# Performance work log

Measured on AMD Instinct MI355X. Metric: run time of the kernel, lower is better.

Reference implementation:

```python
import jax, jax.numpy as jnp
import numpy as np

N_NODES = 50000
N_EDGES = 800000
IN_DIM = 128
HID = 256
BN_EPS = 1e-5
NEG_SLOPE = 0.01


def setup_inputs() -> dict:
    key = jax.random.key(0)
    ks = jax.random.split(key, 8)
    inp = {
        "x": jax.random.normal(ks[0], (N_NODES, IN_DIM), dtype=jnp.float32),
        "src": jax.random.randint(ks[1], (N_EDGES,), 0, N_NODES, dtype=jnp.int32),
        "dst": jax.random.randint(ks[2], (N_EDGES,), 0, N_NODES, dtype=jnp.int32),
        # layer 0 MLP (in->hid->hid) + BN params
        "w1_0": jax.random.normal(ks[3], (IN_DIM, HID), dtype=jnp.float32) / np.sqrt(IN_DIM),
        "b1_0": jnp.zeros((HID,), jnp.float32),
        "w2_0": jax.random.normal(ks[4], (HID, HID), dtype=jnp.float32) / np.sqrt(HID),
        "b2_0": jnp.zeros((HID,), jnp.float32),
        "g0": jnp.ones((HID,), jnp.float32),
        "be0": jnp.zeros((HID,), jnp.float32),
        "m0": jnp.zeros((HID,), jnp.float32),
        "v0": jnp.ones((HID,), jnp.float32),
        # layers 1..2 stacked (hid->hid->hid) + BN params
        "w1_r": jax.random.normal(ks[5], (2, HID, HID), dtype=jnp.float32) / np.sqrt(HID),
        "b1_r": jnp.zeros((2, HID), jnp.float32),
        "w2_r": jax.random.normal(ks[6], (2, HID, HID), dtype=jnp.float32) / np.sqrt(HID),
        "b2_r": jnp.zeros((2, HID), jnp.float32),
        "g_r": jnp.ones((2, HID), jnp.float32),
        "be_r": jnp.zeros((2, HID), jnp.float32),
        "m_r": jnp.zeros((2, HID), jnp.float32),
        "v_r": jnp.ones((2, HID), jnp.float32),
    }
    return inp


def _gin_layer(h, src, dst, w1, b1, w2, b2, g, be, m, v, last):
    # GINConv (eps=0): (1+eps)*h + sum_{j in N(i)} h_j  via gather + scatter-add
    agg = jax.ops.segment_sum(h[src], dst, num_segments=N_NODES)
    z = h + agg
    # 2-layer MLP (dropout is identity in eval)
    z = jax.nn.leaky_relu(z @ w1 + b1, NEG_SLOPE)
    z = z @ w2 + b2
    # BatchNorm1d (eval: running stats)
    z = (z - m) * jax.lax.rsqrt(v + BN_EPS) * g + be
    if not last:
        z = jax.nn.leaky_relu(z, NEG_SLOPE)
    return z


def reference(x, src, dst, w1_0, b1_0, w2_0, b2_0, g0, be0, m0, v0,
              w1_r, b1_r, w2_r, b2_r, g_r, be_r, m_r, v_r):
    h = _gin_layer(x, src, dst, w1_0, b1_0, w2_0, b2_0, g0, be0, m0, v0, last=False)
    for l in range(2):
        h = _gin_layer(h, src, dst, w1_r[l], b1_r[l], w2_r[l], b2_r[l],
                       g_r[l], be_r[l], m_r[l], v_r[l], last=(l == 1))
    return h
```

## Files before the change

### kernel.cpp

```cpp
#include <hip/hip_runtime.h>
#include <hip/hip_bf16.h>
#include <stdint.h>

#define NN 50000
#define NE 800000
#define IND 128
#define HID 256
#define MPAD 50048
#define NBLK 49

#define NCH 64
#define CHSZ 12500
#define NRG 8
#define RGSZ 6250

typedef unsigned int uint32;
typedef unsigned short ushort_t;
typedef __attribute__((ext_vector_type(8))) short short8;
typedef __attribute__((ext_vector_type(4))) float f32x4;

typedef const __attribute__((address_space(1))) void* gptr_t;
typedef __attribute__((address_space(3))) void* lptr_t;

__device__ __forceinline__ ushort_t f2b(float f) {
  uint32 u = __float_as_uint(f);
  u = (u + 0x7fffu + ((u >> 16) & 1u)) >> 16;
  return (ushort_t)u;
}
__device__ __forceinline__ float blo(uint32 u) { return __uint_as_float(u << 16); }
__device__ __forceinline__ float bhi(uint32 u) { return __uint_as_float(u & 0xffff0000u); }
__device__ __forceinline__ uint32 pack2(float a, float b) {
  return (uint32)f2b(a) | ((uint32)f2b(b) << 16);
}

__global__ __launch_bounds__(256) void histp_k(const int* __restrict__ dst,
                                               uint32* __restrict__ partial,
                                               int* __restrict__ rnk) {
  __shared__ uint32 lh[RGSZ];
  const int c = blockIdx.x & (NCH - 1);
  const int rg = blockIdx.x >> 6;
  const int r0 = rg * RGSZ;
  for (int i = threadIdx.x; i < RGSZ; i += 256) lh[i] = 0;
  __syncthreads();
  const int e0 = c * CHSZ;
  for (int i = threadIdx.x; i < CHSZ; i += 256) {
    int e = e0 + i;
    int d = dst[e] - r0;
    if ((unsigned)d < (unsigned)RGSZ) rnk[e] = (int)atomicAdd(&lh[d], 1u);
  }
  __syncthreads();
  uint32* po = partial + (size_t)c * NN + r0;
  for (int i = threadIdx.x; i < RGSZ; i += 256) po[i] = lh[i];
}

__global__ void coff_k(uint32* __restrict__ partial, int* __restrict__ cnt) {
  int bin = blockIdx.x * 256 + threadIdx.x;
  if (bin >= NN) return;
  uint32 run = 0;
#pragma unroll
  for (int c = 0; c < NCH; c++) {
    uint32 t = partial[(size_t)c * NN + bin];
    partial[(size_t)c * NN + bin] = run;
    run += t;
  }
  cnt[bin] = (int)run;
}

__global__ void bsum_k(const int* __restrict__ cnt, int* __restrict__ bsum) {
  __shared__ int ws[16];
  const int tid = threadIdx.x, ln = tid & 63, wv = tid >> 6;
  int i = blockIdx.x * 1024 + tid;
  int v = (i < NN) ? cnt[i] : 0;
#pragma unroll
  for (int d = 32; d; d >>= 1) v += __shfl_down(v, d, 64);
  if (ln == 0) ws[wv] = v;
  __syncthreads();
  if (tid < 16) {
    int s = ws[tid];
#pragma unroll
    for (int d = 8; d; d >>= 1) s += __shfl_down(s, d, 64);
    if (tid == 0) bsum[blockIdx.x] = s;
  }
}

__global__ void bscan_k(int* __restrict__ bsum, int* __restrict__ rp) {
  int tid = threadIdx.x;
  int v = (tid < NBLK) ? bsum[tid] : 0;
  int x = v;
#pragma unroll
  for (int d = 1; d < 64; d <<= 1) {
    int t = __shfl_up(x, d, 64);
    if (tid >= d) x += t;
  }
  if (tid < NBLK) bsum[tid] = x - v;
  if (tid == 0) rp[NN] = NE;
}

__global__ void scan2_k(const int* __restrict__ cnt, const int* __restrict__ bsum,
                        int* __restrict__ rp) {
  __shared__ int ws[16];
  const int tid = threadIdx.x, ln = tid & 63, wv = tid >> 6;
  int i = blockIdx.x * 1024 + tid;
  int v = (i < NN) ? cnt[i] : 0;
  int x = v;
#pragma unroll
  for (int d = 1; d < 64; d <<= 1) {
    int t = __shfl_up(x, d, 64);
    if (ln >= d) x += t;
  }
  if (ln == 63) ws[wv] = x;
  __syncthreads();
  if (tid < 16) {
    int s = ws[tid];
#pragma unroll
    for (int d = 1; d < 16; d <<= 1) {
      int t = __shfl_up(s, d, 64);
      if (tid >= d) s += t;
    }
    ws[tid] = s;
  }
  __syncthreads();
  int excl = x - v + (wv ? ws[wv - 1] : 0) + bsum[blockIdx.x];
  if (i < NN) rp[i] = excl;
}

__global__ void scat2_k(const int* __restrict__ src, const int* __restrict__ dst,
                        const int* __restrict__ rp, const uint32* __restrict__ partial,
                        const int* __restrict__ rnk, int* __restrict__ esrc) {
  int e = blockIdx.x * 256 + threadIdx.x;
  if (e < NE) {
    int d = dst[e];
    int c = e / CHSZ;
    int pos = rp[d] + (int)partial[(size_t)c * NN + d] + rnk[e];
    esrc[pos] = src[e];
  }
}

__global__ void prep_k(const float* __restrict__ w1_0, const float* __restrict__ w2_0,
                       const float* __restrict__ w1_r, const float* __restrict__ w2_r,
                       const float* b1_0, const float* b2_0, const float* g0,
                       const float* be0, const float* m0, const float* v0,
                       const float* b1_r, const float* b2_r, const float* g_r,
                       const float* be_r, const float* m_r, const float* v_r,
                       ushort_t* __restrict__ wt,
                       float* bi1, float* sc2, float* bi2) {
  const int which = blockIdx.y;
  if (which < 6) {
    const int n = blockIdx.x, k = threadIdx.x;
    const float* w; ushort_t* o; int K = HID;
    switch (which) {
      case 0: w = w1_0; o = wt; K = IND; break;
      case 1: w = w2_0; o = wt + HID * IND; break;
      case 2: w = w1_r; o = wt + HID * IND + 1 * HID * HID; break;
      case 3: w = w2_r; o = wt + HID * IND + 2 * HID * HID; break;
      case 4: w = w1_r + HID * HID; o = wt + HID * IND + 3 * HID * HID; break;
      default: w = w2_r + HID * HID; o = wt + HID * IND + 4 * HID * HID; break;
    }
    if (k < K) o[n * K + k] = f2b(w[(size_t)k * HID + n]);
  } else {
    const int l = blockIdx.x;
    if (l >= 3) return;
    const int j = threadIdx.x;
    float b1, b2, g, be, m, v;
    if (l == 0) { b1 = b1_0[j]; b2 = b2_0[j]; g = g0[j]; be = be0[j]; m = m0[j]; v = v0[j]; }
    else { int o = (l - 1) * HID + j; b1 = b1_r[o]; b2 = b2_r[o]; g = g_r[o]; be = be_r[o]; m = m_r[o]; v = v_r[o]; }
    int o = l * HID + j;
    bi1[o] = b1;
    float s = g * rsqrtf(v + 1e-5f);
    sc2[o] = s;
    bi2[o] = (b2 - m) * s + be;
  }
}

__global__ void x2b_k(const float* __restrict__ x, ushort_t* __restrict__ xb) {
  int i = blockIdx.x * 256 + threadIdx.x;
  const int n = NN * IND / 2;
  if (i < n) {
    float2 f = ((const float2*)x)[i];
    ((uint32*)xb)[i] = pack2(f.x, f.y);
  }
}

__global__ void agg256_k(const ushort_t* __restrict__ h, const int* __restrict__ rp,
                         const int* __restrict__ esrc, ushort_t* __restrict__ z) {
  int wid = threadIdx.x >> 6, lane = threadIdx.x & 63;
  int node = blockIdx.x * 4 + wid;
  if (node >= NN) return;
  const uint2* hp = (const uint2*)h;
  uint2 v = hp[(size_t)node * 64 + lane];
  float a0 = blo(v.x), a1 = bhi(v.x), a2 = blo(v.y), a3 = bhi(v.y);
  int e0 = rp[node], e1 = rp[node + 1];
  int e = e0;
  for (; e + 8 <= e1; e += 8) {
    int s[8];
#pragma unroll
    for (int q = 0; q < 8; q++) s[q] = esrc[e + q];
    uint2 u[8];
#pragma unroll
    for (int q = 0; q < 8; q++) u[q] = hp[(size_t)s[q] * 64 + lane];
#pragma unroll
    for (int q = 0; q < 8; q++) {
      a0 += blo(u[q].x); a1 += bhi(u[q].x); a2 += blo(u[q].y); a3 += bhi(u[q].y);
    }
  }
  for (; e < e1; e++) {
    int s = esrc[e];
    uint2 u = hp[(size_t)s * 64 + lane];
    a0 += blo(u.x); a1 += bhi(u.x); a2 += blo(u.y); a3 += bhi(u.y);
  }
  uint2 o; o.x = pack2(a0, a1); o.y = pack2(a2, a3);
  ((uint2*)z)[(size_t)node * 64 + lane] = o;
}

__global__ void agg128_k(const ushort_t* __restrict__ h, const int* __restrict__ rp,
                         const int* __restrict__ esrc, ushort_t* __restrict__ z) {
  int wid = threadIdx.x >> 6, lane = threadIdx.x & 63;
  int node = blockIdx.x * 4 + wid;
  if (node >= NN) return;
  const uint32* hp = (const uint32*)h;
  uint32 v = hp[(size_t)node * 64 + lane];
  float a0 = blo(v), a1 = bhi(v);
  int e0 = rp[node], e1 = rp[node + 1];
  int e = e0;
  for (; e + 8 <= e1; e += 8) {
    int s[8];
#pragma unroll
    for (int q = 0; q < 8; q++) s[q] = esrc[e + q];
    uint32 u[8];
#pragma unroll
    for (int q = 0; q < 8; q++) u[q] = hp[(size_t)s[q] * 64 + lane];
#pragma unroll
    for (int q = 0; q < 8; q++) { a0 += blo(u[q]); a1 += bhi(u[q]); }
  }
  for (; e < e1; e++) {
    int s = esrc[e];
    uint32 u = hp[(size_t)s * 64 + lane];
    a0 += blo(u); a1 += bhi(u);
  }
  ((uint32*)z)[(size_t)node * 64 + lane] = pack2(a0, a1);
}

template<int K1>
__global__ __launch_bounds__(256, 2) void fgemm_k(
    const ushort_t* __restrict__ A, const ushort_t* __restrict__ B1t,
    const ushort_t* __restrict__ B2t, const float* __restrict__ bi1,
    const float* __restrict__ sc2, const float* __restrict__ bi2,
    void* __restrict__ out, int lrelu2, int f32out) {
  __shared__ ushort_t As[2][64 * 32];
  __shared__ ushort_t Bs[2][256 * 32];
  __shared__ ushort_t C1s[64 * 264];
  const int tid = threadIdx.x;
  const int lane = tid & 63;
  const int wid = tid >> 6;
  const int m0 = blockIdx.x * 64;
  const int srow = tid >> 2;
  const int sch = (tid & 3) * 8;
  const int fr = lane & 15;
  const int fk = (lane >> 4) * 8;
  const int er = lane >> 4;
  const int ec = lane & 15;
  constexpr int T1 = K1 / 32;

  auto stage1 = [&](int b, int kk) {
    __builtin_amdgcn_global_load_lds((gptr_t)(A + (size_t)(m0 + srow) * K1 + kk + sch),
                                     (lptr_t)(&As[b][srow * 32 + sch]), 16, 0, 0);
#pragma unroll
    for (int p = 0; p < 4; p++)
      __builtin_amdgcn_global_load_lds(
          (gptr_t)(B1t + (size_t)(p * 64 + srow) * K1 + kk + sch),
          (lptr_t)(&Bs[b][(p * 64 + srow) * 32 + sch]), 16, 0, 0);
  };
  auto stage2 = [&](int b, int kk) {
#pragma unroll
    for (int p = 0; p < 4; p++)
      __builtin_amdgcn_global_load_lds(
          (gptr_t)(B2t + (size_t)(p * 64 + srow) * HID + kk + sch),
          (lptr_t)(&Bs[b][(p * 64 + srow) * 32 + sch]), 16, 0, 0);
  };

  f32x4 zero = {0.f, 0.f, 0.f, 0.f};
  f32x4 acc[4][4];
#pragma unroll
  for (int i = 0; i < 4; i++)
#pragma unroll
    for (int j = 0; j < 4; j++) acc[i][j] = zero;

  stage1(0, 0);
  __syncthreads();
#pragma unroll 2
  for (int t = 0; t < T1; t++) {
    const int b = t & 1;
    if (t + 1 < T1) stage1(b ^ 1, (t + 1) * 32);
    short8 af[4], bfv[4];
#pragma unroll
    for (int i = 0; i < 4; i++)
      af[i] = *(const short8*)(&As[b][(i * 16 + fr) * 32 + fk]);
#pragma unroll
    for (int j = 0; j < 4; j++)
      bfv[j] = *(const short8*)(&Bs[b][(wid * 64 + j * 16 + fr) * 32 + fk]);
#pragma unroll
    for (int i = 0; i < 4; i++)
#pragma unroll
      for (int j = 0; j < 4; j++)
        acc[i][j] = __builtin_amdgcn_mfma_f32_16x16x32_bf16(af[i], bfv[j], acc[i][j], 0, 0, 0);
    __syncthreads();
  }

  stage2(0, 0);

#pragma unroll
  for (int j = 0; j < 4; j++) {
    int col = wid * 64 + j * 16 + ec;
    float b = bi1[col];
#pragma unroll
    for (int i = 0; i < 4; i++) {
#pragma unroll
      for (int r = 0; r < 4; r++) {
        int row = i * 16 + er * 4 + r;
        float v = acc[i][j][r] + b;
        v = (v > 0.f) ? v : 0.01f * v;
        C1s[row * 264 + col] = f2b(v);
      }
    }
  }
  __syncthreads();

  f32x4 acc2[4][4];
#pragma unroll
  for (int i = 0; i < 4; i++)
#pragma unroll
    for (int j = 0; j < 4; j++) acc2[i][j] = zero;

#pragma unroll 2
  for (int t = 0; t < 8; t++) {
    const int b = t & 1;
    if (t + 1 < 8) stage2(b ^ 1, (t + 1) * 32);
    const int kk = t * 32;
    short8 af[4], bfv[4];
#pragma unroll
    for (int i = 0; i < 4; i++)
      af[i] = *(const short8*)(C1s + (i * 16 + fr) * 264 + kk + fk);
#pragma unroll
    for (int j = 0; j < 4; j++)
      bfv[j] = *(const short8*)(&Bs[b][(wid * 64 + j * 16 + fr) * 32 + fk]);
#pragma unroll
    for (int i = 0; i < 4; i++)
#pragma unroll
      for (int j = 0; j < 4; j++)
        acc2[i][j] = __builtin_amdgcn_mfma_f32_16x16x32_bf16(af[i], bfv[j], acc2[i][j], 0, 0, 0);
    __syncthreads();
  }

#pragma unroll
  for (int j = 0; j < 4; j++) {
    int col = wid * 64 + j * 16 + ec;
    float s = sc2[col], b = bi2[col];
#pragma unroll
    for (int i = 0; i < 4; i++) {
#pragma unroll
      for (int r = 0; r < 4; r++) {
        int row = m0 + i * 16 + er * 4 + r;
        float v = acc2[i][j][r] * s + b;
        if (lrelu2) v = (v > 0.f) ? v : 0.01f * v;
        if (row < NN) {
          if (f32out) ((float*)out)[(size_t)row * HID + col] = v;
          else        ((ushort_t*)out)[(size_t)row * HID + col] = f2b(v);
        }
      }
    }
  }
}

extern "C" void kernel_launch(void* const* d_in, const int* in_sizes, int n_in,
                              void* d_out, int out_size, void* d_ws, size_t ws_size,
                              hipStream_t stream) {
  const float* x    = (const float*)d_in[0];
  const int*   src  = (const int*)d_in[1];
  const int*   dst  = (const int*)d_in[2];
  const float* w1_0 = (const float*)d_in[3];
  const float* b1_0 = (const float*)d_in[4];
  const float* w2_0 = (const float*)d_in[5];
  const float* b2_0 = (const float*)d_in[6];
  const float* g0   = (const float*)d_in[7];
  const float* be0  = (const float*)d_in[8];
  const float* m0   = (const float*)d_in[9];
  const float* v0   = (const float*)d_in[10];
  const float* w1_r = (const float*)d_in[11];
  const float* b1_r = (const float*)d_in[12];
  const float* w2_r = (const float*)d_in[13];
  const float* b2_r = (const float*)d_in[14];
  const float* g_r  = (const float*)d_in[15];
  const float* be_r = (const float*)d_in[16];
  const float* m_r  = (const float*)d_in[17];
  const float* v_r  = (const float*)d_in[18];

  char* ws = (char*)d_ws;
  size_t off = 0;
  auto alloc = [&](size_t bytes) {
    void* p = ws + off;
    off = (off + bytes + 255) & ~(size_t)255;
    return p;
  };
  ushort_t* bufA  = (ushort_t*)alloc((size_t)MPAD * HID * 2);
  ushort_t* bufB  = (ushort_t*)alloc((size_t)MPAD * HID * 2);
  ushort_t* xb    = (ushort_t*)alloc((size_t)MPAD * IND * 2);
  int*      rp    = (int*)alloc((NN + 1) * sizeof(int));
  int*      cnt   = (int*)alloc(NN * sizeof(int));
  int*      bsum  = (int*)alloc(NBLK * sizeof(int));
  int*      esrc  = (int*)alloc((size_t)NE * sizeof(int));
  ushort_t* wt    = (ushort_t*)alloc(((size_t)HID * IND + 5 * (size_t)HID * HID) * 2);
  float*    bi1   = (float*)alloc(3 * HID * sizeof(float));
  float*    sc2   = (float*)alloc(3 * HID * sizeof(float));
  float*    bi2   = (float*)alloc(3 * HID * sizeof(float));
  (void)ws_size; (void)in_sizes; (void)n_in; (void)out_size;

  uint32* partial = (uint32*)bufA;
  int*    rnk     = (int*)bufB;

  ushort_t* w1_0t = wt;
  ushort_t* w2_0t = wt + HID * IND;
  ushort_t* w1r0t = wt + HID * IND + 1 * HID * HID;
  ushort_t* w2r0t = wt + HID * IND + 2 * HID * HID;
  ushort_t* w1r1t = wt + HID * IND + 3 * HID * HID;
  ushort_t* w2r1t = wt + HID * IND + 4 * HID * HID;

  histp_k<<<NCH * NRG, 256, 0, stream>>>(dst, partial, rnk);
  coff_k<<<(NN + 255) / 256, 256, 0, stream>>>(partial, cnt);
  bsum_k<<<NBLK, 1024, 0, stream>>>(cnt, bsum);
  bscan_k<<<1, 64, 0, stream>>>(bsum, rp);
  scan2_k<<<NBLK, 1024, 0, stream>>>(cnt, bsum, rp);
  scat2_k<<<(NE + 255) / 256, 256, 0, stream>>>(src, dst, rp, partial, rnk, esrc);

  prep_k<<<dim3(HID, 7), 256, 0, stream>>>(w1_0, w2_0, w1_r, w2_r,
                                           b1_0, b2_0, g0, be0, m0, v0,
                                           b1_r, b2_r, g_r, be_r, m_r, v_r,
                                           wt, bi1, sc2, bi2);
  x2b_k<<<(NN * IND / 2 + 255) / 256, 256, 0, stream>>>(x, xb);

  const int GG = MPAD / 64;
  agg128_k<<<NN / 4, 256, 0, stream>>>(xb, rp, esrc, bufA);
  fgemm_k<IND><<<GG, 256, 0, stream>>>(bufA, w1_0t, w2_0t, bi1, sc2, bi2, bufB, 1, 0);
  agg256_k<<<NN / 4, 256, 0, stream>>>(bufB, rp, esrc, bufA);
  fgemm_k<HID><<<GG, 256, 0, stream>>>(bufA, w1r0t, w2r0t, bi1 + HID, sc2 + HID, bi2 + HID, bufB, 1, 0);
  agg256_k<<<NN / 4, 256, 0, stream>>>(bufB, rp, esrc, bufA);
  fgemm_k<HID><<<GG, 256, 0, stream>>>(bufA, w1r1t, w2r1t, bi1 + 2 * HID, sc2 + 2 * HID, bi2 + 2 * HID, d_out, 0, 1);
}
```

Measured before the change: 458.6 us.

## Pre-pack weights into MFMA fragment order and load operands directly from global

Weight transposes are now written in a layout matching the per-lane MFMA B-fragment order, so each wave can fetch its B fragments with one coalesced 16-byte load per lane. The double-buffered LDS staging of A and B tiles, with its barriers, is removed, and A fragments are read straight from global memory. This cuts LDS traffic and per-iteration synchronisation. In exchange it relies on L1/L2 caching for the weights and A rows reused across the four waves, and it loses the explicit prefetch overlap.

```diff
diff --git a/kernel.cpp b/kernel.cpp
--- a/kernel.cpp
+++ b/kernel.cpp
@@ -19,9 +19,6 @@
 typedef __attribute__((ext_vector_type(8))) short short8;
 typedef __attribute__((ext_vector_type(4))) float f32x4;
 
-typedef const __attribute__((address_space(1))) void* gptr_t;
-typedef __attribute__((address_space(3))) void* lptr_t;
-
 __device__ __forceinline__ ushort_t f2b(float f) {
   uint32 u = __float_as_uint(f);
   u = (u + 0x7fffu + ((u >> 16) & 1u)) >> 16;
@@ -31,6 +28,12 @@
 __device__ __forceinline__ float bhi(uint32 u) { return __uint_as_float(u & 0xffff0000u); }
 __device__ __forceinline__ uint32 pack2(float a, float b) {
   return (uint32)f2b(a) | ((uint32)f2b(b) << 16);
+}
+
+__device__ __forceinline__ int packidx(int col, int k, int Kd) {
+  int lane = ((k & 31) >> 3) * 16 + (col & 15);
+  int c = (((col >> 6) * (Kd >> 5) + (k >> 5)) * 4 + ((col >> 4) & 3)) * 64 + lane;
+  return c * 8 + (k & 7);
 }
 
 __global__ __launch_bounds__(256) void histp_k(const int* __restrict__ dst,
@@ -156,7 +159,7 @@
       case 4: w = w1_r + HID * HID; o = wt + HID * IND + 3 * HID * HID; break;
       default: w = w2_r + HID * HID; o = wt + HID * IND + 4 * HID * HID; break;
     }
-    if (k < K) o[n * K + k] = f2b(w[(size_t)k * HID + n]);
+    if (k < K) o[packidx(n, k, K)] = f2b(w[(size_t)k * HID + n]);
   } else {
     const int l = blockIdx.x;
     if (l >= 3) return;
@@ -246,37 +249,19 @@
     const ushort_t* __restrict__ B2t, const float* __restrict__ bi1,
     const float* __restrict__ sc2, const float* __restrict__ bi2,
     void* __restrict__ out, int lrelu2, int f32out) {
-  __shared__ ushort_t As[2][64 * 32];
-  __shared__ ushort_t Bs[2][256 * 32];
   __shared__ ushort_t C1s[64 * 264];
   const int tid = threadIdx.x;
   const int lane = tid & 63;
   const int wid = tid >> 6;
   const int m0 = blockIdx.x * 64;
-  const int srow = tid >> 2;
-  const int sch = (tid & 3) * 8;
   const int fr = lane & 15;
   const int fk = (lane >> 4) * 8;
   const int er = lane >> 4;
   const int ec = lane & 15;
-  constexpr int T1 = K1 / 32;
-
-  auto stage1 = [&](int b, int kk) {
-    __builtin_amdgcn_global_load_lds((gptr_t)(A + (size_t)(m0 + srow) * K1 + kk + sch),
-                                     (lptr_t)(&As[b][srow * 32 + sch]), 16, 0, 0);
-#pragma unroll
-    for (int p = 0; p < 4; p++)
-      __builtin_amdgcn_global_load_lds(
-          (gptr_t)(B1t + (size_t)(p * 64 + srow) * K1 + kk + sch),
-          (lptr_t)(&Bs[b][(p * 64 + srow) * 32 + sch]), 16, 0, 0);
-  };
-  auto stage2 = [&](int b, int kk) {
-#pragma unroll
-    for (int p = 0; p < 4; p++)
-      __builtin_amdgcn_global_load_lds(
-          (gptr_t)(B2t + (size_t)(p * 64 + srow) * HID + kk + sch),
-          (lptr_t)(&Bs[b][(p * 64 + srow) * 32 + sch]), 16, 0, 0);
-  };
+  constexpr int S1 = K1 / 32;
+
+  const short8* Bp1 = (const short8*)B1t;
+  const short8* Bp2 = (const short8*)B2t;
 
   f32x4 zero = {0.f, 0.f, 0.f, 0.f};
   f32x4 acc[4][4];
@@ -285,28 +270,22 @@
 #pragma unroll
     for (int j = 0; j < 4; j++) acc[i][j] = zero;
 
-  stage1(0, 0);
-  __syncthreads();
 #pragma unroll 2
-  for (int t = 0; t < T1; t++) {
-    const int b = t & 1;
-    if (t + 1 < T1) stage1(b ^ 1, (t + 1) * 32);
+  for (int ks = 0; ks < S1; ks++) {
+    const int kk = ks * 32;
     short8 af[4], bfv[4];
 #pragma unroll
     for (int i = 0; i < 4; i++)
-      af[i] = *(const short8*)(&As[b][(i * 16 + fr) * 32 + fk]);
+      af[i] = *(const short8*)(A + (size_t)(m0 + i * 16 + fr) * K1 + kk + fk);
 #pragma unroll
     for (int j = 0; j < 4; j++)
-      bfv[j] = *(const short8*)(&Bs[b][(wid * 64 + j * 16 + fr) * 32 + fk]);
+      bfv[j] = Bp1[((wid * S1 + ks) * 4 + j) * 64 + lane];
 #pragma unroll
     for (int i = 0; i < 4; i++)
 #pragma unroll
       for (int j = 0; j < 4; j++)
         acc[i][j] = __builtin_amdgcn_mfma_f32_16x16x32_bf16(af[i], bfv[j], acc[i][j], 0, 0, 0);
-    __syncthreads();
-  }
-
-  stage2(0, 0);
+  }
 
 #pragma unroll
   for (int j = 0; j < 4; j++) {
@@ -332,23 +311,20 @@
     for (int j = 0; j < 4; j++) acc2[i][j] = zero;
 
 #pragma unroll 2
-  for (int t = 0; t < 8; t++) {
-    const int b = t & 1;
-    if (t + 1 < 8) stage2(b ^ 1, (t + 1) * 32);
-    const int kk = t * 32;
+  for (int ks = 0; ks < 8; ks++) {
+    const int kk = ks * 32;
     short8 af[4], bfv[4];
 #pragma unroll
     for (int i = 0; i < 4; i++)
       af[i] = *(const short8*)(C1s + (i * 16 + fr) * 264 + kk + fk);
 #pragma unroll
     for (int j = 0; j < 4; j++)
-      bfv[j] = *(const short8*)(&Bs[b][(wid * 64 + j * 16 + fr) * 32 + fk]);
+      bfv[j] = Bp2[((wid * 8 + ks) * 4 + j) * 64 + lane];
 #pragma unroll
     for (int i = 0; i < 4; i++)
 #pragma unroll
       for (int j = 0; j < 4; j++)
         acc2[i][j] = __builtin_amdgcn_mfma_f32_16x16x32_bf16(af[i], bfv[j], acc2[i][j], 0, 0, 0);
-    __syncthreads();
   }
 
 #pragma unroll
```

Measured after the change: 433.4 us. -5.5%, faster.
